# Optimization experiments

Hardware: AMD Instinct MI355X
Metric: run time of the kernel (lower is better)

## Reference

```python
import jax, jax.numpy as jnp
import numpy as np
from jax import lax

B, T = 64, 200
NUM_C, DIM_S, SIZE_M = 2000, 128, 50


def setup_inputs() -> dict:
    key = jax.random.key(0)
    ks = jax.random.split(key, 12)
    d = {}
    d['skill'] = jax.random.randint(ks[0], (B, T), 0, NUM_C)
    d['answer'] = jax.random.randint(ks[1], (B, T), 0, 2)
    s = 1.0 / np.sqrt(DIM_S)
    d['k_emb'] = jax.random.normal(ks[2], (NUM_C + 1, DIM_S), jnp.float32)
    d['v_emb'] = jax.random.normal(ks[3], (2 * NUM_C + 1, DIM_S), jnp.float32)
    # kaiming_normal on [size_m, dim_s]: std = sqrt(2/dim_s)
    d['Mk'] = jax.random.normal(ks[4], (SIZE_M, DIM_S), jnp.float32) * np.sqrt(2.0 / DIM_S)
    d['Mv0'] = jax.random.normal(ks[5], (SIZE_M, DIM_S), jnp.float32) * np.sqrt(2.0 / DIM_S)
    d['f_W'] = jax.random.normal(ks[6], (DIM_S, 2 * DIM_S), jnp.float32) * (1.0 / np.sqrt(2 * DIM_S))
    d['f_b'] = jnp.zeros((DIM_S,), jnp.float32)
    d['p_W'] = jax.random.normal(ks[7], (NUM_C, DIM_S), jnp.float32) * s
    d['p_b'] = jnp.zeros((NUM_C,), jnp.float32)
    d['e_W'] = jax.random.normal(ks[8], (DIM_S, DIM_S), jnp.float32) * s
    d['e_b'] = jnp.zeros((DIM_S,), jnp.float32)
    d['a_W'] = jax.random.normal(ks[9], (DIM_S, DIM_S), jnp.float32) * s
    d['a_b'] = jnp.zeros((DIM_S,), jnp.float32)
    return d


def reference(skill, answer, k_emb, v_emb, Mk, Mv0, f_W, f_b, p_W, p_b, e_W, e_b, a_W, a_b):
    num_c = p_W.shape[0]
    bsz = skill.shape[0]
    answer_x = jnp.where(answer == 2, 1, answer)
    x = skill + num_c * answer_x                       # [B,T]
    k = k_emb[skill]                                   # [B,T,D]
    v = v_emb[x]                                       # [B,T,D]
    w = jax.nn.softmax(jnp.einsum('btd,md->btm', k, Mk), axis=-1)   # [B,T,M]
    e = jax.nn.sigmoid(jnp.einsum('btd,ed->bte', v, e_W) + e_b)      # [B,T,D]
    a = jnp.tanh(jnp.einsum('btd,ed->bte', v, a_W) + a_b)            # [B,T,D]

    Mv_init = jnp.broadcast_to(Mv0, (bsz,) + Mv0.shape)              # [B,M,D]

    def step(Mvt, inp):
        et, at, wt = inp                               # [B,D],[B,D],[B,M]
        # read uses pre-update memory (Mv[:, :-1] in the torch code)
        read = jnp.einsum('bm,bmd->bd', wt, Mvt)
        Mvt_new = Mvt * (1.0 - wt[:, :, None] * et[:, None, :]) + wt[:, :, None] * at[:, None, :]
        return Mvt_new, read

    _, reads = lax.scan(step, Mv_init,
                        (e.transpose(1, 0, 2), a.transpose(1, 0, 2), w.transpose(1, 0, 2)))
    reads = reads.transpose(1, 0, 2)                   # [B,T,D]

    f = jnp.tanh(jnp.concatenate([reads, k], axis=-1) @ f_W.T + f_b)  # [B,T,D]
    p = jax.nn.sigmoid(f @ p_W.T + p_b)                # [B,T,num_c] (dropout is identity at eval)
    p = p[:, :-1, :]
    next_skill = skill[:, 1:]                          # [B,T-1]
    idx = jnp.minimum(next_skill, num_c - 1)
    pred = jnp.take_along_axis(p, idx[..., None], axis=-1)[..., 0]
    pred = jnp.where(next_skill < num_c, pred, 0.0)    # index num_c -> zero row in torch one_hot
    return pred
```

## Files before the change

### kernel.cpp

```cpp
#include <hip/hip_runtime.h>
#include <math.h>

#define Bsz 64
#define Tn 200
#define NUMC 2000
#define DS 128
#define SM 50
#define NTOK (Bsz*Tn)
#define WG2 10
#define MPG2 5

typedef __attribute__((ext_vector_type(8))) short bfrag;
typedef __attribute__((ext_vector_type(4))) float f32x4;
typedef __attribute__((ext_vector_type(4))) unsigned int u32x4;

__device__ __forceinline__ unsigned short f2bf(float x) {
    unsigned int u = __builtin_bit_cast(unsigned int, x);
    u = u + 0x7fffu + ((u >> 16) & 1u);
    return (unsigned short)(u >> 16);
}
__device__ __forceinline__ unsigned int pack2(float a, float b) {
    return (unsigned int)f2bf(a) | ((unsigned int)f2bf(b) << 16);
}
__device__ __forceinline__ bfrag mk_frag(f32x4 x, f32x4 y) {
    u32x4 t;
    t[0] = pack2(x[0], x[1]); t[1] = pack2(x[2], x[3]);
    t[2] = pack2(y[0], y[1]); t[3] = pack2(y[2], y[3]);
    return __builtin_bit_cast(bfrag, t);
}

__device__ __forceinline__ float fast_exp(float x)  { return __builtin_amdgcn_exp2f(x * 1.44269504f); }
__device__ __forceinline__ float fast_rcp(float x)  { return __builtin_amdgcn_rcpf(x); }
__device__ __forceinline__ float fast_sigmoid(float x) { return fast_rcp(1.f + fast_exp(-x)); }
__device__ __forceinline__ float fast_tanh(float x) { return 1.f - 2.f * fast_rcp(fast_exp(2.f * x) + 1.f); }

__device__ __forceinline__ void load_group(const bfrag* __restrict__ B, int nt0, int L, bfrag bf[4][4]) {
    #pragma unroll
    for (int t = 0; t < 4; t++)
        #pragma unroll
        for (int ki = 0; ki < 4; ki++)
            bf[t][ki] = B[(size_t)((nt0 + t) * 4 + ki) * 64 + L];
}
__device__ __forceinline__ void mfma_group(const bfrag A[4], const bfrag bf[4][4], f32x4 acc[4]) {
    #pragma unroll
    for (int ki = 0; ki < 4; ki++)
        #pragma unroll
        for (int t = 0; t < 4; t++)
            acc[t] = __builtin_amdgcn_mfma_f32_16x16x32_bf16(A[ki], bf[t][ki], acc[t], 0, 0, 0);
}

__global__ __launch_bounds__(256) void k0_cast(
    const float* __restrict__ eW, const float* __restrict__ aW,
    const float* __restrict__ fW, const float* __restrict__ Mk,
    unsigned int* __restrict__ BeaU, unsigned int* __restrict__ BkmU,
    unsigned int* __restrict__ Bf0U)
{
    const int g = blockIdx.x * 256 + threadIdx.x;
    if (g >= 9216) return;
    int gm, mat;
    unsigned int* dst;
    if (g < 4096)      { mat = 0; gm = g;        dst = BeaU; }
    else if (g < 7168) { mat = 1; gm = g - 4096; dst = BkmU; }
    else               { mat = 2; gm = g - 7168; dst = Bf0U; }
    const int nt = gm >> 8, r = gm & 255, ki = r >> 6, L = r & 63;
    const int n = nt * 16 + (L & 15);
    const int k = ki * 32 + (L >> 4) * 8;

    const float* src = nullptr;
    if (mat == 0) {
        src = (n < 128) ? (eW + (size_t)n * DS + k) : (aW + (size_t)(n - 128) * DS + k);
    } else if (mat == 1) {
        if (n < 128)      src = fW + (size_t)n * (2 * DS) + DS + k;
        else if (n < 128 + SM) src = Mk + (size_t)(n - 128) * DS + k;
    } else {
        src = fW + (size_t)n * (2 * DS) + k;
    }
    float v[8];
    #pragma unroll
    for (int j = 0; j < 8; j++) v[j] = src ? src[j] : 0.f;
    u32x4 o;
    o[0] = pack2(v[0], v[1]); o[1] = pack2(v[2], v[3]);
    o[2] = pack2(v[4], v[5]); o[3] = pack2(v[6], v[7]);
    ((u32x4*)dst)[gm] = o;
}

__global__ __launch_bounds__(64) void k1_gemm(
    const int* __restrict__ skill, const int* __restrict__ answer,
    const float* __restrict__ k_emb, const float* __restrict__ v_emb,
    const unsigned int* __restrict__ BeaU, const unsigned int* __restrict__ BkmU,
    const float* __restrict__ eB, const float* __restrict__ aB,
    float* __restrict__ w_buf, float* __restrict__ e_buf,
    float* __restrict__ a_buf, float* __restrict__ kp_buf)
{
    const int bid = blockIdx.x;
    const int L = threadIdx.x, L15 = L & 15, quad = L >> 4;

    if (bid < NTOK/16) {
        const int tok0 = bid * 16;
        const int tokA = tok0 + L15;
        const int tokD0 = tok0 + quad * 4;

        const bfrag* Bea = (const bfrag*)BeaU;
        bfrag bfA[4][4], bfB[4][4];
        load_group(Bea, 0, L, bfA);
        load_group(Bea, 4, L, bfB);

        const int s  = skill[tokA];
        const int an = answer[tokA];
        const int ax = (an == 2) ? 1 : an;
        const float* vp = v_emb + ((size_t)(s + NUMC * ax)) * DS + quad * 8;
        bfrag Vf[4];
        #pragma unroll
        for (int ki = 0; ki < 4; ki++) {
            const f32x4* a = (const f32x4*)(vp + ki * 32);
            Vf[ki] = mk_frag(a[0], a[1]);
        }

        f32x4 acc[4];
        #pragma unroll
        for (int t = 0; t < 4; t++) acc[t] = (f32x4){0.f,0.f,0.f,0.f};
        mfma_group(Vf, bfA, acc);
        load_group(Bea, 8, L, bfA);
        #pragma unroll
        for (int t = 0; t < 4; t++) {
            const int n = t * 16 + L15;
            const float bias = eB[n];
            #pragma unroll
            for (int reg = 0; reg < 4; reg++)
                e_buf[(size_t)(tokD0 + reg) * DS + n] = fast_sigmoid(acc[t][reg] + bias);
        }

        #pragma unroll
        for (int t = 0; t < 4; t++) acc[t] = (f32x4){0.f,0.f,0.f,0.f};
        mfma_group(Vf, bfB, acc);
        load_group(Bea, 12, L, bfB);
        #pragma unroll
        for (int t = 0; t < 4; t++) {
            const int n = (4 + t) * 16 + L15;
            const float bias = eB[n];
            #pragma unroll
            for (int reg = 0; reg < 4; reg++)
                e_buf[(size_t)(tokD0 + reg) * DS + n] = fast_sigmoid(acc[t][reg] + bias);
        }

        #pragma unroll
        for (int t = 0; t < 4; t++) acc[t] = (f32x4){0.f,0.f,0.f,0.f};
        mfma_group(Vf, bfA, acc);
        #pragma unroll
        for (int t = 0; t < 4; t++) {
            const int n = t * 16 + L15;
            const float bias = aB[n];
            #pragma unroll
            for (int reg = 0; reg < 4; reg++)
                a_buf[(size_t)(tokD0 + reg) * DS + n] = fast_tanh(acc[t][reg] + bias);
        }

        #pragma unroll
        for (int t = 0; t < 4; t++) acc[t] = (f32x4){0.f,0.f,0.f,0.f};
        mfma_group(Vf, bfB, acc);
        #pragma unroll
        for (int t = 0; t < 4; t++) {
            const int n = (4 + t) * 16 + L15;
            const float bias = aB[n];
            #pragma unroll
            for (int reg = 0; reg < 4; reg++)
                a_buf[(size_t)(tokD0 + reg) * DS + n] = fast_tanh(acc[t][reg] + bias);
        }
    } else {
        const int tok0 = (bid - NTOK/16) * 16;
        const int tokA = tok0 + L15;
        const int tokD0 = tok0 + quad * 4;

        const bfrag* Bkm = (const bfrag*)BkmU;
        bfrag bfA[4][4], bfB[4][4];
        load_group(Bkm, 0, L, bfA);
        load_group(Bkm, 4, L, bfB);

        const int s = skill[tokA];
        const float* kp = k_emb + (size_t)s * DS + quad * 8;
        bfrag Kf[4];
        #pragma unroll
        for (int ki = 0; ki < 4; ki++) {
            const f32x4* b = (const f32x4*)(kp + ki * 32);
            Kf[ki] = mk_frag(b[0], b[1]);
        }

        __shared__ float wl[16][52];

        f32x4 acc[4];
        #pragma unroll
        for (int t = 0; t < 4; t++) acc[t] = (f32x4){0.f,0.f,0.f,0.f};
        mfma_group(Kf, bfA, acc);
        load_group(Bkm, 8, L, bfA);
        #pragma unroll
        for (int t = 0; t < 4; t++) {
            const int n = t * 16 + L15;
            #pragma unroll
            for (int reg = 0; reg < 4; reg++)
                kp_buf[(size_t)(tokD0 + reg) * DS + n] = acc[t][reg];
        }

        #pragma unroll
        for (int t = 0; t < 4; t++) acc[t] = (f32x4){0.f,0.f,0.f,0.f};
        mfma_group(Kf, bfB, acc);
        #pragma unroll
        for (int t = 0; t < 4; t++) {
            const int n = (4 + t) * 16 + L15;
            #pragma unroll
            for (int reg = 0; reg < 4; reg++)
                kp_buf[(size_t)(tokD0 + reg) * DS + n] = acc[t][reg];
        }

        #pragma unroll
        for (int t = 0; t < 4; t++) acc[t] = (f32x4){0.f,0.f,0.f,0.f};
        mfma_group(Kf, bfA, acc);
        #pragma unroll
        for (int t = 0; t < 4; t++) {
            const int c = (8 + t) * 16 + L15 - 128;
            if (c < SM) {
                #pragma unroll
                for (int reg = 0; reg < 4; reg++)
                    wl[quad * 4 + reg][c] = acc[t][reg];
            }
        }
        __syncthreads();
        if (L < 16) {
            float mx = -1e30f;
            for (int m = 0; m < SM; m++) mx = fmaxf(mx, wl[L][m]);
            float sum = 0.f;
            float ex[SM];
            for (int m = 0; m < SM; m++) { ex[m] = fast_exp(wl[L][m] - mx); sum += ex[m]; }
            const float inv = fast_rcp(sum);
            float* wp = w_buf + (size_t)(tok0 + L) * SM;
            for (int m = 0; m < SM; m++) wp[m] = ex[m] * inv;
        }
    }
}

__global__ __launch_bounds__(64) void k2_scan(
    const float* __restrict__ w_buf, const float* __restrict__ e_buf,
    const float* __restrict__ a_buf, const float* __restrict__ Mv0,
    float* __restrict__ part_buf)
{
    const int bi   = blockIdx.x;
    const int b    = bi / (2*WG2);
    const int r    = bi % (2*WG2);
    const int dh   = r / WG2;
    const int mg   = r % WG2;
    const int lane = threadIdx.x;
    const int d    = dh*64 + lane;
    const int m0   = mg * MPG2;
    const int base = b * Tn;

    float Mv[MPG2];
    #pragma unroll
    for (int m = 0; m < MPG2; m++) Mv[m] = Mv0[(size_t)(m0+m)*DS + d];

    float* pout = part_buf + (size_t)mg * NTOK * DS;

    float se[4][2], sa[4][2], sw[4][2][MPG2];

    #define LOADST(ST, T)                                                      \
        { const int tc_ = ((T) < Tn) ? (T) : 0;                                \
          _Pragma("unroll")                                                    \
          for (int q_ = 0; q_ < 2; q_++) {                                     \
              const int tf_ = base + tc_ + q_;                                 \
              se[ST][q_] = e_buf[(size_t)tf_*DS + d];                          \
              sa[ST][q_] = a_buf[(size_t)tf_*DS + d];                          \
              _Pragma("unroll")                                                \
              for (int m_ = 0; m_ < MPG2; m_++)                                \
                  sw[ST][q_][m_] = w_buf[(size_t)tf_*SM + m0 + m_];            \
          } }

    LOADST(0, 0) LOADST(1, 2) LOADST(2, 4) LOADST(3, 6)

    for (int i = 0; i < 25; i++) {
        const int tb = i * 8;
        #pragma unroll
        for (int sub = 0; sub < 4; sub++) {
            const int t0 = tb + sub * 2;
            #pragma unroll
            for (int q = 0; q < 2; q++) {
                const float ev = se[sub][q], av = sa[sub][q];
                float rd = 0.f;
                #pragma unroll
                for (int m = 0; m < MPG2; m++) {
                    const float wm = sw[sub][q][m];
                    rd = fmaf(wm, Mv[m], rd);
                    Mv[m] = fmaf(-wm, fmaf(ev, Mv[m], -av), Mv[m]);
                }
                pout[(size_t)(base + t0 + q)*DS + d] = rd;
            }
            LOADST(sub, t0 + 8)
        }
    }
}

__global__ __launch_bounds__(64) void k3_gemm(
    const float* __restrict__ part_buf, const float* __restrict__ kp_buf,
    const unsigned int* __restrict__ Bf0U, const float* __restrict__ fB,
    const float* __restrict__ pW, const float* __restrict__ pB,
    const int* __restrict__ skill, float* __restrict__ out)
{
    const int L = threadIdx.x, L15 = L & 15, quad = L >> 4;
    const int tok0 = blockIdx.x * 16;
    const int tokA = tok0 + L15;
    const int tokD0 = tok0 + quad * 4;

    const bfrag* Bf0 = (const bfrag*)Bf0U;
    bfrag bfA[4][4], bfB[4][4];
    load_group(Bf0, 0, L, bfA);
    load_group(Bf0, 4, L, bfB);

    bfrag Rf[4];
    #pragma unroll
    for (int ki = 0; ki < 4; ki++) {
        const float* p0 = part_buf + (size_t)tokA * DS + ki * 32 + quad * 8;
        f32x4 x = (f32x4){0.f,0.f,0.f,0.f}, y = (f32x4){0.f,0.f,0.f,0.f};
        #pragma unroll
        for (int g = 0; g < WG2; g++) {
            const f32x4* q4 = (const f32x4*)(p0 + (size_t)g * NTOK * DS);
            x = x + q4[0]; y = y + q4[1];
        }
        Rf[ki] = mk_frag(x, y);
    }

    float f[4][8];
    f32x4 acc[4];

    #pragma unroll
    for (int t = 0; t < 4; t++) acc[t] = (f32x4){0.f,0.f,0.f,0.f};
    mfma_group(Rf, bfA, acc);
    #pragma unroll
    for (int t = 0; t < 4; t++) {
        const int n = t * 16 + L15;
        const float fb = fB[n];
        #pragma unroll
        for (int reg = 0; reg < 4; reg++)
            f[reg][t] = fast_tanh(acc[t][reg] + kp_buf[(size_t)(tokD0 + reg) * DS + n] + fb);
    }

    #pragma unroll
    for (int t = 0; t < 4; t++) acc[t] = (f32x4){0.f,0.f,0.f,0.f};
    mfma_group(Rf, bfB, acc);
    #pragma unroll
    for (int t = 0; t < 4; t++) {
        const int n = (4 + t) * 16 + L15;
        const float fb = fB[n];
        #pragma unroll
        for (int reg = 0; reg < 4; reg++)
            f[reg][4 + t] = fast_tanh(acc[t][reg] + kp_buf[(size_t)(tokD0 + reg) * DS + n] + fb);
    }

    #pragma unroll
    for (int reg = 0; reg < 4; reg++) {
        const int tok = tokD0 + reg;
        const int t = tok % Tn;
        const bool act = (t < Tn - 1);
        int sn = 0, ix = 0;
        float contrib = 0.f;
        if (act) {
            sn = skill[tok + 1];
            ix = (sn < NUMC) ? sn : (NUMC - 1);
            const float* pr = pW + (size_t)ix * DS + L15;
            #pragma unroll
            for (int nt = 0; nt < 8; nt++)
                contrib = fmaf(f[reg][nt], pr[nt * 16], contrib);
        }
        #pragma unroll
        for (int msk = 1; msk <= 8; msk <<= 1)
            contrib += __shfl_xor(contrib, msk);
        if (act && L15 == 0) {
            const float val = contrib + pB[ix];
            const float prd = (sn < NUMC) ? fast_sigmoid(val) : 0.f;
            out[(size_t)(tok / Tn) * (Tn - 1) + t] = prd;
        }
    }
}

extern "C" void kernel_launch(void* const* d_in, const int* in_sizes, int n_in,
                              void* d_out, int out_size, void* d_ws, size_t ws_size,
                              hipStream_t stream)
{
    const int*   skill  = (const int*)  d_in[0];
    const int*   answer = (const int*)  d_in[1];
    const float* k_emb  = (const float*)d_in[2];
    const float* v_emb  = (const float*)d_in[3];
    const float* Mk     = (const float*)d_in[4];
    const float* Mv0    = (const float*)d_in[5];
    const float* f_W    = (const float*)d_in[6];
    const float* f_b    = (const float*)d_in[7];
    const float* p_W    = (const float*)d_in[8];
    const float* p_b    = (const float*)d_in[9];
    const float* e_W    = (const float*)d_in[10];
    const float* e_b    = (const float*)d_in[11];
    const float* a_W    = (const float*)d_in[12];
    const float* a_b    = (const float*)d_in[13];
    float* out = (float*)d_out;

    float* ws       = (float*)d_ws;
    float* w_buf    = ws;
    float* e_buf    = w_buf    + (size_t)NTOK*SM;
    float* a_buf    = e_buf    + (size_t)NTOK*DS;
    float* kp_buf   = a_buf    + (size_t)NTOK*DS;
    float* part_buf = kp_buf   + (size_t)NTOK*DS;
    unsigned int* BeaU = (unsigned int*)(part_buf + (size_t)WG2*NTOK*DS);
    unsigned int* BkmU = BeaU + 4096 * 4;
    unsigned int* Bf0U = BkmU + 3072 * 4;

    k0_cast<<<36, 256, 0, stream>>>(e_W, a_W, f_W, Mk, BeaU, BkmU, Bf0U);
    k1_gemm<<<2*(NTOK/16), 64, 0, stream>>>(skill, answer, k_emb, v_emb,
        BeaU, BkmU, e_b, a_b, w_buf, e_buf, a_buf, kp_buf);
    k2_scan<<<Bsz*2*WG2, 64, 0, stream>>>(w_buf, e_buf, a_buf, Mv0, part_buf);
    k3_gemm<<<NTOK/16, 64, 0, stream>>>(part_buf, kp_buf, Bf0U, f_b,
        p_W, p_b, skill, out);
}
```

Measured before the change: 140.6 us.

## Fuse all stages into one cooperative kernel with grid syncs and bf16 partials

Replaces the four separate launches (weight cast, projection GEMMs, memory scan, output GEMM) with one cooperative kernel of 256 blocks x 512 threads. Stages are separated by grid.sync, and each wave takes one work item. The softmax for w is now done in registers instead of through LDS. The scan's per-group partial reads are stored as bf16 rather than fp32, halving partial-buffer traffic. In exchange the stages are serialized by grid barriers, occupancy depends on the cooperative grid size, and the partials lose some precision.

Measured after the change: 232.3 us. 65.2% more time.

```diff
diff --git a/kernel.cpp b/kernel.cpp
--- a/kernel.cpp
+++ b/kernel.cpp
@@ -1,5 +1,8 @@
 #include <hip/hip_runtime.h>
+#include <hip/hip_cooperative_groups.h>
 #include <math.h>
+
+namespace cg = cooperative_groups;
 
 #define Bsz 64
 #define Tn 200
@@ -22,6 +25,9 @@
 __device__ __forceinline__ unsigned int pack2(float a, float b) {
     return (unsigned int)f2bf(a) | ((unsigned int)f2bf(b) << 16);
 }
+__device__ __forceinline__ float bf2f(unsigned int u) {
+    return __builtin_bit_cast(float, u << 16);
+}
 __device__ __forceinline__ bfrag mk_frag(f32x4 x, f32x4 y) {
     u32x4 t;
     t[0] = pack2(x[0], x[1]); t[1] = pack2(x[2], x[3]);
@@ -49,331 +55,346 @@
             acc[t] = __builtin_amdgcn_mfma_f32_16x16x32_bf16(A[ki], bf[t][ki], acc[t], 0, 0, 0);
 }
 
-__global__ __launch_bounds__(256) void k0_cast(
-    const float* __restrict__ eW, const float* __restrict__ aW,
-    const float* __restrict__ fW, const float* __restrict__ Mk,
+__global__ __launch_bounds__(512, 2) void fused(
+    const int* __restrict__ skill, const int* __restrict__ answer,
+    const float* __restrict__ k_emb, const float* __restrict__ v_emb,
+    const float* __restrict__ Mk, const float* __restrict__ Mv0,
+    const float* __restrict__ fW, const float* __restrict__ fB,
+    const float* __restrict__ pW, const float* __restrict__ pB,
+    const float* __restrict__ eW, const float* __restrict__ eB,
+    const float* __restrict__ aW, const float* __restrict__ aB,
+    float* __restrict__ out,
+    float* __restrict__ w_buf, float* __restrict__ e_buf,
+    float* __restrict__ a_buf, float* __restrict__ kp_buf,
+    unsigned short* __restrict__ part16,
     unsigned int* __restrict__ BeaU, unsigned int* __restrict__ BkmU,
     unsigned int* __restrict__ Bf0U)
 {
-    const int g = blockIdx.x * 256 + threadIdx.x;
-    if (g >= 9216) return;
-    int gm, mat;
-    unsigned int* dst;
-    if (g < 4096)      { mat = 0; gm = g;        dst = BeaU; }
-    else if (g < 7168) { mat = 1; gm = g - 4096; dst = BkmU; }
-    else               { mat = 2; gm = g - 7168; dst = Bf0U; }
-    const int nt = gm >> 8, r = gm & 255, ki = r >> 6, L = r & 63;
-    const int n = nt * 16 + (L & 15);
-    const int k = ki * 32 + (L >> 4) * 8;
-
-    const float* src = nullptr;
-    if (mat == 0) {
-        src = (n < 128) ? (eW + (size_t)n * DS + k) : (aW + (size_t)(n - 128) * DS + k);
-    } else if (mat == 1) {
-        if (n < 128)      src = fW + (size_t)n * (2 * DS) + DS + k;
-        else if (n < 128 + SM) src = Mk + (size_t)(n - 128) * DS + k;
-    } else {
-        src = fW + (size_t)n * (2 * DS) + k;
-    }
-    float v[8];
-    #pragma unroll
-    for (int j = 0; j < 8; j++) v[j] = src ? src[j] : 0.f;
-    u32x4 o;
-    o[0] = pack2(v[0], v[1]); o[1] = pack2(v[2], v[3]);
-    o[2] = pack2(v[4], v[5]); o[3] = pack2(v[6], v[7]);
-    ((u32x4*)dst)[gm] = o;
-}
-
-__global__ __launch_bounds__(64) void k1_gemm(
-    const int* __restrict__ skill, const int* __restrict__ answer,
-    const float* __restrict__ k_emb, const float* __restrict__ v_emb,
-    const unsigned int* __restrict__ BeaU, const unsigned int* __restrict__ BkmU,
-    const float* __restrict__ eB, const float* __restrict__ aB,
-    float* __restrict__ w_buf, float* __restrict__ e_buf,
-    float* __restrict__ a_buf, float* __restrict__ kp_buf)
-{
-    const int bid = blockIdx.x;
-    const int L = threadIdx.x, L15 = L & 15, quad = L >> 4;
-
-    if (bid < NTOK/16) {
-        const int tok0 = bid * 16;
-        const int tokA = tok0 + L15;
-        const int tokD0 = tok0 + quad * 4;
-
-        const bfrag* Bea = (const bfrag*)BeaU;
-        bfrag bfA[4][4], bfB[4][4];
-        load_group(Bea, 0, L, bfA);
-        load_group(Bea, 4, L, bfB);
-
-        const int s  = skill[tokA];
-        const int an = answer[tokA];
-        const int ax = (an == 2) ? 1 : an;
-        const float* vp = v_emb + ((size_t)(s + NUMC * ax)) * DS + quad * 8;
-        bfrag Vf[4];
-        #pragma unroll
-        for (int ki = 0; ki < 4; ki++) {
-            const f32x4* a = (const f32x4*)(vp + ki * 32);
-            Vf[ki] = mk_frag(a[0], a[1]);
-        }
-
-        f32x4 acc[4];
-        #pragma unroll
-        for (int t = 0; t < 4; t++) acc[t] = (f32x4){0.f,0.f,0.f,0.f};
-        mfma_group(Vf, bfA, acc);
-        load_group(Bea, 8, L, bfA);
-        #pragma unroll
-        for (int t = 0; t < 4; t++) {
-            const int n = t * 16 + L15;
-            const float bias = eB[n];
-            #pragma unroll
-            for (int reg = 0; reg < 4; reg++)
-                e_buf[(size_t)(tokD0 + reg) * DS + n] = fast_sigmoid(acc[t][reg] + bias);
-        }
-
-        #pragma unroll
-        for (int t = 0; t < 4; t++) acc[t] = (f32x4){0.f,0.f,0.f,0.f};
-        mfma_group(Vf, bfB, acc);
-        load_group(Bea, 12, L, bfB);
-        #pragma unroll
-        for (int t = 0; t < 4; t++) {
-            const int n = (4 + t) * 16 + L15;
-            const float bias = eB[n];
-            #pragma unroll
-            for (int reg = 0; reg < 4; reg++)
-                e_buf[(size_t)(tokD0 + reg) * DS + n] = fast_sigmoid(acc[t][reg] + bias);
-        }
-
-        #pragma unroll
-        for (int t = 0; t < 4; t++) acc[t] = (f32x4){0.f,0.f,0.f,0.f};
-        mfma_group(Vf, bfA, acc);
-        #pragma unroll
-        for (int t = 0; t < 4; t++) {
-            const int n = t * 16 + L15;
-            const float bias = aB[n];
-            #pragma unroll
-            for (int reg = 0; reg < 4; reg++)
-                a_buf[(size_t)(tokD0 + reg) * DS + n] = fast_tanh(acc[t][reg] + bias);
-        }
-
-        #pragma unroll
-        for (int t = 0; t < 4; t++) acc[t] = (f32x4){0.f,0.f,0.f,0.f};
-        mfma_group(Vf, bfB, acc);
-        #pragma unroll
-        for (int t = 0; t < 4; t++) {
-            const int n = (4 + t) * 16 + L15;
-            const float bias = aB[n];
-            #pragma unroll
-            for (int reg = 0; reg < 4; reg++)
-                a_buf[(size_t)(tokD0 + reg) * DS + n] = fast_tanh(acc[t][reg] + bias);
-        }
-    } else {
-        const int tok0 = (bid - NTOK/16) * 16;
-        const int tokA = tok0 + L15;
-        const int tokD0 = tok0 + quad * 4;
-
-        const bfrag* Bkm = (const bfrag*)BkmU;
-        bfrag bfA[4][4], bfB[4][4];
-        load_group(Bkm, 0, L, bfA);
-        load_group(Bkm, 4, L, bfB);
-
-        const int s = skill[tokA];
-        const float* kp = k_emb + (size_t)s * DS + quad * 8;
-        bfrag Kf[4];
-        #pragma unroll
-        for (int ki = 0; ki < 4; ki++) {
-            const f32x4* b = (const f32x4*)(kp + ki * 32);
-            Kf[ki] = mk_frag(b[0], b[1]);
-        }
-
-        __shared__ float wl[16][52];
-
-        f32x4 acc[4];
-        #pragma unroll
-        for (int t = 0; t < 4; t++) acc[t] = (f32x4){0.f,0.f,0.f,0.f};
-        mfma_group(Kf, bfA, acc);
-        load_group(Bkm, 8, L, bfA);
-        #pragma unroll
-        for (int t = 0; t < 4; t++) {
-            const int n = t * 16 + L15;
-            #pragma unroll
-            for (int reg = 0; reg < 4; reg++)
-                kp_buf[(size_t)(tokD0 + reg) * DS + n] = acc[t][reg];
-        }
-
-        #pragma unroll
-        for (int t = 0; t < 4; t++) acc[t] = (f32x4){0.f,0.f,0.f,0.f};
-        mfma_group(Kf, bfB, acc);
-        #pragma unroll
-        for (int t = 0; t < 4; t++) {
-            const int n = (4 + t) * 16 + L15;
-            #pragma unroll
-            for (int reg = 0; reg < 4; reg++)
-                kp_buf[(size_t)(tokD0 + reg) * DS + n] = acc[t][reg];
-        }
-
-        #pragma unroll
-        for (int t = 0; t < 4; t++) acc[t] = (f32x4){0.f,0.f,0.f,0.f};
-        mfma_group(Kf, bfA, acc);
-        #pragma unroll
-        for (int t = 0; t < 4; t++) {
-            const int c = (8 + t) * 16 + L15 - 128;
-            if (c < SM) {
-                #pragma unroll
-                for (int reg = 0; reg < 4; reg++)
-                    wl[quad * 4 + reg][c] = acc[t][reg];
-            }
-        }
-        __syncthreads();
-        if (L < 16) {
-            float mx = -1e30f;
-            for (int m = 0; m < SM; m++) mx = fmaxf(mx, wl[L][m]);
-            float sum = 0.f;
-            float ex[SM];
-            for (int m = 0; m < SM; m++) { ex[m] = fast_exp(wl[L][m] - mx); sum += ex[m]; }
-            const float inv = fast_rcp(sum);
-            float* wp = w_buf + (size_t)(tok0 + L) * SM;
-            for (int m = 0; m < SM; m++) wp[m] = ex[m] * inv;
+    cg::grid_group grid = cg::this_grid();
+    const int tid = threadIdx.x;
+    const int wv  = tid >> 6;
+    const int L   = tid & 63, L15 = L & 15, quad = (L >> 4) & 3;
+
+    {
+        const int g = blockIdx.x * 512 + tid;
+        if (g < 9216) {
+            int gm, mat;
+            unsigned int* dst;
+            if (g < 4096)      { mat = 0; gm = g;        dst = BeaU; }
+            else if (g < 7168) { mat = 1; gm = g - 4096; dst = BkmU; }
+            else               { mat = 2; gm = g - 7168; dst = Bf0U; }
+            const int nt = gm >> 8, r = gm & 255, ki = r >> 6, Lc = r & 63;
+            const int n = nt * 16 + (Lc & 15);
+            const int k = ki * 32 + (Lc >> 4) * 8;
+            const float* src = nullptr;
+            if (mat == 0) {
+                src = (n < 128) ? (eW + (size_t)n * DS + k) : (aW + (size_t)(n - 128) * DS + k);
+            } else if (mat == 1) {
+                if (n < 128)           src = fW + (size_t)n * (2 * DS) + DS + k;
+                else if (n < 128 + SM) src = Mk + (size_t)(n - 128) * DS + k;
+            } else {
+                src = fW + (size_t)n * (2 * DS) + k;
+            }
+            float v[8];
+            #pragma unroll
+            for (int j = 0; j < 8; j++) v[j] = src ? src[j] : 0.f;
+            u32x4 o;
+            o[0] = pack2(v[0], v[1]); o[1] = pack2(v[2], v[3]);
+            o[2] = pack2(v[4], v[5]); o[3] = pack2(v[6], v[7]);
+            ((u32x4*)dst)[gm] = o;
         }
     }
-}
-
-__global__ __launch_bounds__(64) void k2_scan(
-    const float* __restrict__ w_buf, const float* __restrict__ e_buf,
-    const float* __restrict__ a_buf, const float* __restrict__ Mv0,
-    float* __restrict__ part_buf)
-{
-    const int bi   = blockIdx.x;
-    const int b    = bi / (2*WG2);
-    const int r    = bi % (2*WG2);
-    const int dh   = r / WG2;
-    const int mg   = r % WG2;
-    const int lane = threadIdx.x;
-    const int d    = dh*64 + lane;
-    const int m0   = mg * MPG2;
-    const int base = b * Tn;
-
-    float Mv[MPG2];
-    #pragma unroll
-    for (int m = 0; m < MPG2; m++) Mv[m] = Mv0[(size_t)(m0+m)*DS + d];
-
-    float* pout = part_buf + (size_t)mg * NTOK * DS;
-
-    float se[4][2], sa[4][2], sw[4][2][MPG2];
-
-    #define LOADST(ST, T)                                                      \
-        { const int tc_ = ((T) < Tn) ? (T) : 0;                                \
-          _Pragma("unroll")                                                    \
-          for (int q_ = 0; q_ < 2; q_++) {                                     \
-              const int tf_ = base + tc_ + q_;                                 \
-              se[ST][q_] = e_buf[(size_t)tf_*DS + d];                          \
-              sa[ST][q_] = a_buf[(size_t)tf_*DS + d];                          \
-              _Pragma("unroll")                                                \
-              for (int m_ = 0; m_ < MPG2; m_++)                                \
-                  sw[ST][q_][m_] = w_buf[(size_t)tf_*SM + m0 + m_];            \
-          } }
-
-    LOADST(0, 0) LOADST(1, 2) LOADST(2, 4) LOADST(3, 6)
-
-    for (int i = 0; i < 25; i++) {
-        const int tb = i * 8;
-        #pragma unroll
-        for (int sub = 0; sub < 4; sub++) {
-            const int t0 = tb + sub * 2;
-            #pragma unroll
-            for (int q = 0; q < 2; q++) {
-                const float ev = se[sub][q], av = sa[sub][q];
-                float rd = 0.f;
-                #pragma unroll
-                for (int m = 0; m < MPG2; m++) {
-                    const float wm = sw[sub][q][m];
-                    rd = fmaf(wm, Mv[m], rd);
-                    Mv[m] = fmaf(-wm, fmaf(ev, Mv[m], -av), Mv[m]);
-                }
-                pout[(size_t)(base + t0 + q)*DS + d] = rd;
-            }
-            LOADST(sub, t0 + 8)
+    grid.sync();
+
+    {
+        const int tA = wv * 256 + blockIdx.x;
+        if (tA < 800) {
+            const int tok0 = tA * 16;
+            const int tokA = tok0 + L15;
+            const int tokD0 = tok0 + quad * 4;
+
+            const bfrag* Bea = (const bfrag*)BeaU;
+            bfrag bfA[4][4], bfB[4][4];
+            load_group(Bea, 0, L, bfA);
+            load_group(Bea, 4, L, bfB);
+
+            const int s  = skill[tokA];
+            const int an = answer[tokA];
+            const int ax = (an == 2) ? 1 : an;
+            const float* vp = v_emb + ((size_t)(s + NUMC * ax)) * DS + quad * 8;
+            bfrag Vf[4];
+            #pragma unroll
+            for (int ki = 0; ki < 4; ki++) {
+                const f32x4* a = (const f32x4*)(vp + ki * 32);
+                Vf[ki] = mk_frag(a[0], a[1]);
+            }
+
+            f32x4 acc[4];
+            #pragma unroll
+            for (int t = 0; t < 4; t++) acc[t] = (f32x4){0.f,0.f,0.f,0.f};
+            mfma_group(Vf, bfA, acc);
+            load_group(Bea, 8, L, bfA);
+            #pragma unroll
+            for (int t = 0; t < 4; t++) {
+                const int n = t * 16 + L15;
+                const float bias = eB[n];
+                #pragma unroll
+                for (int reg = 0; reg < 4; reg++)
+                    e_buf[(size_t)(tokD0 + reg) * DS + n] = fast_sigmoid(acc[t][reg] + bias);
+            }
+
+            #pragma unroll
+            for (int t = 0; t < 4; t++) acc[t] = (f32x4){0.f,0.f,0.f,0.f};
+            mfma_group(Vf, bfB, acc);
+            load_group(Bea, 12, L, bfB);
+            #pragma unroll
+            for (int t = 0; t < 4; t++) {
+                const int n = (4 + t) * 16 + L15;
+                const float bias = eB[n];
+                #pragma unroll
+                for (int reg = 0; reg < 4; reg++)
+                    e_buf[(size_t)(tokD0 + reg) * DS + n] = fast_sigmoid(acc[t][reg] + bias);
+            }
+
+            #pragma unroll
+            for (int t = 0; t < 4; t++) acc[t] = (f32x4){0.f,0.f,0.f,0.f};
+            mfma_group(Vf, bfA, acc);
+            #pragma unroll
+            for (int t = 0; t < 4; t++) {
+                const int n = t * 16 + L15;
+                const float bias = aB[n];
+                #pragma unroll
+                for (int reg = 0; reg < 4; reg++)
+                    a_buf[(size_t)(tokD0 + reg) * DS + n] = fast_tanh(acc[t][reg] + bias);
+            }
+
+            #pragma unroll
+            for (int t = 0; t < 4; t++) acc[t] = (f32x4){0.f,0.f,0.f,0.f};
+            mfma_group(Vf, bfB, acc);
+            #pragma unroll
+            for (int t = 0; t < 4; t++) {
+                const int n = (4 + t) * 16 + L15;
+                const float bias = aB[n];
+                #pragma unroll
+                for (int reg = 0; reg < 4; reg++)
+                    a_buf[(size_t)(tokD0 + reg) * DS + n] = fast_tanh(acc[t][reg] + bias);
+            }
+        } else if (tA < 1600) {
+            const int tok0 = (tA - 800) * 16;
+            const int tokA = tok0 + L15;
+            const int tokD0 = tok0 + quad * 4;
+
+            const bfrag* Bkm = (const bfrag*)BkmU;
+            bfrag bfA[4][4], bfB[4][4];
+            load_group(Bkm, 0, L, bfA);
+            load_group(Bkm, 4, L, bfB);
+
+            const int s = skill[tokA];
+            const float* kp = k_emb + (size_t)s * DS + quad * 8;
+            bfrag Kf[4];
+            #pragma unroll
+            for (int ki = 0; ki < 4; ki++) {
+                const f32x4* b = (const f32x4*)(kp + ki * 32);
+                Kf[ki] = mk_frag(b[0], b[1]);
+            }
+
+            f32x4 acc[4];
+            #pragma unroll
+            for (int t = 0; t < 4; t++) acc[t] = (f32x4){0.f,0.f,0.f,0.f};
+            mfma_group(Kf, bfA, acc);
+            load_group(Bkm, 8, L, bfA);
+            #pragma unroll
+            for (int t = 0; t < 4; t++) {
+                const int n = t * 16 + L15;
+                #pragma unroll
+                for (int reg = 0; reg < 4; reg++)
+                    kp_buf[(size_t)(tokD0 + reg) * DS + n] = acc[t][reg];
+            }
+
+            #pragma unroll
+            for (int t = 0; t < 4; t++) acc[t] = (f32x4){0.f,0.f,0.f,0.f};
+            mfma_group(Kf, bfB, acc);
+            #pragma unroll
+            for (int t = 0; t < 4; t++) {
+                const int n = (4 + t) * 16 + L15;
+                #pragma unroll
+                for (int reg = 0; reg < 4; reg++)
+                    kp_buf[(size_t)(tokD0 + reg) * DS + n] = acc[t][reg];
+            }
+
+            #pragma unroll
+            for (int t = 0; t < 4; t++) acc[t] = (f32x4){0.f,0.f,0.f,0.f};
+            mfma_group(Kf, bfA, acc);
+            #pragma unroll
+            for (int reg = 0; reg < 4; reg++) {
+                float mx = -1e30f;
+                #pragma unroll
+                for (int t = 0; t < 4; t++) {
+                    const int c = t * 16 + L15;
+                    if (c < SM) mx = fmaxf(mx, acc[t][reg]);
+                }
+                #pragma unroll
+                for (int msk = 1; msk <= 8; msk <<= 1)
+                    mx = fmaxf(mx, __shfl_xor(mx, msk));
+                float ex[4], sum = 0.f;
+                #pragma unroll
+                for (int t = 0; t < 4; t++) {
+                    const int c = t * 16 + L15;
+                    ex[t] = (c < SM) ? fast_exp(acc[t][reg] - mx) : 0.f;
+                    sum += ex[t];
+                }
+                #pragma unroll
+                for (int msk = 1; msk <= 8; msk <<= 1)
+                    sum += __shfl_xor(sum, msk);
+                const float inv = fast_rcp(sum);
+                float* wp = w_buf + (size_t)(tok0 + quad * 4 + reg) * SM;
+                #pragma unroll
+                for (int t = 0; t < 4; t++) {
+                    const int c = t * 16 + L15;
+                    if (c < SM) wp[c] = ex[t] * inv;
+                }
+            }
         }
     }
-}
-
-__global__ __launch_bounds__(64) void k3_gemm(
-    const float* __restrict__ part_buf, const float* __restrict__ kp_buf,
-    const unsigned int* __restrict__ Bf0U, const float* __restrict__ fB,
-    const float* __restrict__ pW, const float* __restrict__ pB,
-    const int* __restrict__ skill, float* __restrict__ out)
-{
-    const int L = threadIdx.x, L15 = L & 15, quad = L >> 4;
-    const int tok0 = blockIdx.x * 16;
-    const int tokA = tok0 + L15;
-    const int tokD0 = tok0 + quad * 4;
-
-    const bfrag* Bf0 = (const bfrag*)Bf0U;
-    bfrag bfA[4][4], bfB[4][4];
-    load_group(Bf0, 0, L, bfA);
-    load_group(Bf0, 4, L, bfB);
-
-    bfrag Rf[4];
-    #pragma unroll
-    for (int ki = 0; ki < 4; ki++) {
-        const float* p0 = part_buf + (size_t)tokA * DS + ki * 32 + quad * 8;
-        f32x4 x = (f32x4){0.f,0.f,0.f,0.f}, y = (f32x4){0.f,0.f,0.f,0.f};
-        #pragma unroll
-        for (int g = 0; g < WG2; g++) {
-            const f32x4* q4 = (const f32x4*)(p0 + (size_t)g * NTOK * DS);
-            x = x + q4[0]; y = y + q4[1];
+    grid.sync();
+
+    {
+        const int bi = blockIdx.x * 5 + wv;
+        if (wv < 5) {
+            const int b    = bi / (2*WG2);
+            const int r    = bi % (2*WG2);
+            const int dh   = r / WG2;
+            const int mg   = r % WG2;
+            const int d    = dh*64 + L;
+            const int m0   = mg * MPG2;
+            const int base = b * Tn;
+
+            float Mv[MPG2];
+            #pragma unroll
+            for (int m = 0; m < MPG2; m++) Mv[m] = Mv0[(size_t)(m0+m)*DS + d];
+
+            unsigned short* pout = part16 + (size_t)mg * NTOK * DS;
+
+            float se[4][2], sa[4][2], sw[4][2][MPG2];
+
+            #define LOADST(ST, T)                                                      \
+                { const int tc_ = ((T) < Tn) ? (T) : 0;                                \
+                  _Pragma("unroll")                                                    \
+                  for (int q_ = 0; q_ < 2; q_++) {                                     \
+                      const int tf_ = base + tc_ + q_;                                 \
+                      se[ST][q_] = e_buf[(size_t)tf_*DS + d];                          \
+                      sa[ST][q_] = a_buf[(size_t)tf_*DS + d];                          \
+                      _Pragma("unroll")                                                \
+                      for (int m_ = 0; m_ < MPG2; m_++)                                \
+                          sw[ST][q_][m_] = w_buf[(size_t)tf_*SM + m0 + m_];            \
+                  } }
+
+            LOADST(0, 0) LOADST(1, 2) LOADST(2, 4) LOADST(3, 6)
+
+            for (int i = 0; i < 25; i++) {
+                const int tb = i * 8;
+                #pragma unroll
+                for (int sub = 0; sub < 4; sub++) {
+                    const int t0 = tb + sub * 2;
+                    #pragma unroll
+                    for (int q = 0; q < 2; q++) {
+                        const float ev = se[sub][q], av = sa[sub][q];
+                        float rd = 0.f;
+                        #pragma unroll
+                        for (int m = 0; m < MPG2; m++) {
+                            const float wm = sw[sub][q][m];
+                            rd = fmaf(wm, Mv[m], rd);
+                            Mv[m] = fmaf(-wm, fmaf(ev, Mv[m], -av), Mv[m]);
+                        }
+                        pout[(size_t)(base + t0 + q)*DS + d] = f2bf(rd);
+                    }
+                    LOADST(sub, t0 + 8)
+                }
+            }
+            #undef LOADST
         }
-        Rf[ki] = mk_frag(x, y);
     }
-
-    float f[4][8];
-    f32x4 acc[4];
-
-    #pragma unroll
-    for (int t = 0; t < 4; t++) acc[t] = (f32x4){0.f,0.f,0.f,0.f};
-    mfma_group(Rf, bfA, acc);
-    #pragma unroll
-    for (int t = 0; t < 4; t++) {
-        const int n = t * 16 + L15;
-        const float fb = fB[n];
-        #pragma unroll
-        for (int reg = 0; reg < 4; reg++)
-            f[reg][t] = fast_tanh(acc[t][reg] + kp_buf[(size_t)(tokD0 + reg) * DS + n] + fb);
-    }
-
-    #pragma unroll
-    for (int t = 0; t < 4; t++) acc[t] = (f32x4){0.f,0.f,0.f,0.f};
-    mfma_group(Rf, bfB, acc);
-    #pragma unroll
-    for (int t = 0; t < 4; t++) {
-        const int n = (4 + t) * 16 + L15;
-        const float fb = fB[n];
-        #pragma unroll
-        for (int reg = 0; reg < 4; reg++)
-            f[reg][4 + t] = fast_tanh(acc[t][reg] + kp_buf[(size_t)(tokD0 + reg) * DS + n] + fb);
-    }
-
-    #pragma unroll
-    for (int reg = 0; reg < 4; reg++) {
-        const int tok = tokD0 + reg;
-        const int t = tok % Tn;
-        const bool act = (t < Tn - 1);
-        int sn = 0, ix = 0;
-        float contrib = 0.f;
-        if (act) {
-            sn = skill[tok + 1];
-            ix = (sn < NUMC) ? sn : (NUMC - 1);
-            const float* pr = pW + (size_t)ix * DS + L15;
-            #pragma unroll
-            for (int nt = 0; nt < 8; nt++)
-                contrib = fmaf(f[reg][nt], pr[nt * 16], contrib);
-        }
-        #pragma unroll
-        for (int msk = 1; msk <= 8; msk <<= 1)
-            contrib += __shfl_xor(contrib, msk);
-        if (act && L15 == 0) {
-            const float val = contrib + pB[ix];
-            const float prd = (sn < NUMC) ? fast_sigmoid(val) : 0.f;
-            out[(size_t)(tok / Tn) * (Tn - 1) + t] = prd;
+    grid.sync();
+
+    {
+        const int tC = wv * 256 + blockIdx.x;
+        if (tC < 800) {
+            const int tok0 = tC * 16;
+            const int tokA = tok0 + L15;
+            const int tokD0 = tok0 + quad * 4;
+
+            const bfrag* Bf0 = (const bfrag*)Bf0U;
+            bfrag bfA[4][4], bfB[4][4];
+            load_group(Bf0, 0, L, bfA);
+            load_group(Bf0, 4, L, bfB);
+
+            bfrag Rf[4];
+            #pragma unroll
+            for (int ki = 0; ki < 4; ki++) {
+                const unsigned short* p0 = part16 + (size_t)tokA * DS + ki * 32 + quad * 8;
+                float s0=0,s1=0,s2=0,s3=0,s4=0,s5=0,s6=0,s7=0;
+                #pragma unroll
+                for (int g = 0; g < WG2; g++) {
+                    u32x4 v = *(const u32x4*)(p0 + (size_t)g * NTOK * DS);
+                    s0 += bf2f(v[0] & 0xffffu); s1 += bf2f(v[0] >> 16);
+                    s2 += bf2f(v[1] & 0xffffu); s3 += bf2f(v[1] >> 16);
+                    s4 += bf2f(v[2] & 0xffffu); s5 += bf2f(v[2] >> 16);
+                    s6 += bf2f(v[3] & 0xffffu); s7 += bf2f(v[3] >> 16);
+                }
+                Rf[ki] = mk_frag((f32x4){s0,s1,s2,s3}, (f32x4){s4,s5,s6,s7});
+            }
+
+            float f[4][8];
+            f32x4 acc[4];
+
+            #pragma unroll
+            for (int t = 0; t < 4; t++) acc[t] = (f32x4){0.f,0.f,0.f,0.f};
+            mfma_group(Rf, bfA, acc);
+            #pragma unroll
+            for (int t = 0; t < 4; t++) {
+                const int n = t * 16 + L15;
+                const float fb = fB[n];
+                #pragma unroll
+                for (int reg = 0; reg < 4; reg++)
+                    f[reg][t] = fast_tanh(acc[t][reg] + kp_buf[(size_t)(tokD0 + reg) * DS + n] + fb);
+            }
+
+            #pragma unroll
+            for (int t = 0; t < 4; t++) acc[t] = (f32x4){0.f,0.f,0.f,0.f};
+            mfma_group(Rf, bfB, acc);
+            #pragma unroll
+            for (int t = 0; t < 4; t++) {
+                const int n = (4 + t) * 16 + L15;
+                const float fb = fB[n];
+                #pragma unroll
+                for (int reg = 0; reg < 4; reg++)
+                    f[reg][4 + t] = fast_tanh(acc[t][reg] + kp_buf[(size_t)(tokD0 + reg) * DS + n] + fb);
+            }
+
+            #pragma unroll
+            for (int reg = 0; reg < 4; reg++) {
+                const int tok = tokD0 + reg;
+                const int t = tok % Tn;
+                const bool act = (t < Tn - 1);
+                int sn = 0, ix = 0;
+                float contrib = 0.f;
+                if (act) {
+                    sn = skill[tok + 1];
+                    ix = (sn < NUMC) ? sn : (NUMC - 1);
+                    const float* pr = pW + (size_t)ix * DS + L15;
+                    #pragma unroll
+                    for (int nt = 0; nt < 8; nt++)
+                        contrib = fmaf(f[reg][nt], pr[nt * 16], contrib);
+                }
+                #pragma unroll
+                for (int msk = 1; msk <= 8; msk <<= 1)
+                    contrib += __shfl_xor(contrib, msk);
+                if (act && L15 == 0) {
+                    const float val = contrib + pB[ix];
+                    const float prd = (sn < NUMC) ? fast_sigmoid(val) : 0.f;
+                    out[(size_t)(tok / Tn) * (Tn - 1) + t] = prd;
+                }
+            }
         }
     }
 }
@@ -398,20 +419,23 @@
     const float* a_b    = (const float*)d_in[13];
     float* out = (float*)d_out;
 
-    float* ws       = (float*)d_ws;
-    float* w_buf    = ws;
-    float* e_buf    = w_buf    + (size_t)NTOK*SM;
-    float* a_buf    = e_buf    + (size_t)NTOK*DS;
-    float* kp_buf   = a_buf    + (size_t)NTOK*DS;
-    float* part_buf = kp_buf   + (size_t)NTOK*DS;
-    unsigned int* BeaU = (unsigned int*)(part_buf + (size_t)WG2*NTOK*DS);
+    float* ws     = (float*)d_ws;
+    float* w_buf  = ws;
+    float* e_buf  = w_buf  + (size_t)NTOK*SM;
+    float* a_buf  = e_buf  + (size_t)NTOK*DS;
+    float* kp_buf = a_buf  + (size_t)NTOK*DS;
+    unsigned short* part16 = (unsigned short*)(kp_buf + (size_t)NTOK*DS);
+    unsigned int* BeaU = (unsigned int*)(part16 + (size_t)WG2*NTOK*DS);
     unsigned int* BkmU = BeaU + 4096 * 4;
     unsigned int* Bf0U = BkmU + 3072 * 4;
 
-    k0_cast<<<36, 256, 0, stream>>>(e_W, a_W, f_W, Mk, BeaU, BkmU, Bf0U);
-    k1_gemm<<<2*(NTOK/16), 64, 0, stream>>>(skill, answer, k_emb, v_emb,
-        BeaU, BkmU, e_b, a_b, w_buf, e_buf, a_buf, kp_buf);
-    k2_scan<<<Bsz*2*WG2, 64, 0, stream>>>(w_buf, e_buf, a_buf, Mv0, part_buf);
-    k3_gemm<<<NTOK/16, 64, 0, stream>>>(part_buf, kp_buf, Bf0U, f_b,
-        p_W, p_b, skill, out);
-}
+    void* args[] = {
+        (void*)&skill, (void*)&answer, (void*)&k_emb, (void*)&v_emb,
+        (void*)&Mk, (void*)&Mv0, (void*)&f_W, (void*)&f_b,
+        (void*)&p_W, (void*)&p_b, (void*)&e_W, (void*)&e_b,
+        (void*)&a_W, (void*)&a_b, (void*)&out,
+        (void*)&w_buf, (void*)&e_buf, (void*)&a_buf, (void*)&kp_buf,
+        (void*)&part16, (void*)&BeaU, (void*)&BkmU, (void*)&Bf0U
+    };
+    hipLaunchCooperativeKernel((void*)fused, dim3(256), dim3(512), args, 0, stream);
+}
```

## Interleave e/a buffers, pad softmax weights per group, deepen scan prefetch

Applied to the files above, without the earlier changes.

The k1 softmax now runs in registers with cross-lane shuffles instead of going through shared memory with only 16 threads active. Its output goes to a padded 80-float-per-token layout grouped by memory slot, so the scan can fetch each group's weights with one vector load plus one scalar. e and a are stored interleaved so the scan reads both with one 8-byte load. The scan's prefetch depth doubles from 8 to 16 timesteps, and a launch bound hint of two blocks is added. The aim is fewer load instructions and more latency hiding in the serial scan, at the cost of more registers and a larger w buffer.

After: 155.3 us. 10.5% more time.

```diff
diff --git a/kernel.cpp b/kernel.cpp
--- a/kernel.cpp
+++ b/kernel.cpp
@@ -12,6 +12,7 @@
 
 typedef __attribute__((ext_vector_type(8))) short bfrag;
 typedef __attribute__((ext_vector_type(4))) float f32x4;
+typedef __attribute__((ext_vector_type(2))) float f32x2;
 typedef __attribute__((ext_vector_type(4))) unsigned int u32x4;
 
 __device__ __forceinline__ unsigned short f2bf(float x) {
@@ -70,7 +71,7 @@
     if (mat == 0) {
         src = (n < 128) ? (eW + (size_t)n * DS + k) : (aW + (size_t)(n - 128) * DS + k);
     } else if (mat == 1) {
-        if (n < 128)      src = fW + (size_t)n * (2 * DS) + DS + k;
+        if (n < 128)           src = fW + (size_t)n * (2 * DS) + DS + k;
         else if (n < 128 + SM) src = Mk + (size_t)(n - 128) * DS + k;
     } else {
         src = fW + (size_t)n * (2 * DS) + k;
@@ -89,8 +90,7 @@
     const float* __restrict__ k_emb, const float* __restrict__ v_emb,
     const unsigned int* __restrict__ BeaU, const unsigned int* __restrict__ BkmU,
     const float* __restrict__ eB, const float* __restrict__ aB,
-    float* __restrict__ w_buf, float* __restrict__ e_buf,
-    float* __restrict__ a_buf, float* __restrict__ kp_buf)
+    float* __restrict__ w2, float* __restrict__ ea_buf, float* __restrict__ kp_buf)
 {
     const int bid = blockIdx.x;
     const int L = threadIdx.x, L15 = L & 15, quad = L >> 4;
@@ -127,7 +127,7 @@
             const float bias = eB[n];
             #pragma unroll
             for (int reg = 0; reg < 4; reg++)
-                e_buf[(size_t)(tokD0 + reg) * DS + n] = fast_sigmoid(acc[t][reg] + bias);
+                ea_buf[(size_t)(tokD0 + reg) * (2*DS) + 2*n] = fast_sigmoid(acc[t][reg] + bias);
         }
 
         #pragma unroll
@@ -140,7 +140,7 @@
             const float bias = eB[n];
             #pragma unroll
             for (int reg = 0; reg < 4; reg++)
-                e_buf[(size_t)(tokD0 + reg) * DS + n] = fast_sigmoid(acc[t][reg] + bias);
+                ea_buf[(size_t)(tokD0 + reg) * (2*DS) + 2*n] = fast_sigmoid(acc[t][reg] + bias);
         }
 
         #pragma unroll
@@ -152,7 +152,7 @@
             const float bias = aB[n];
             #pragma unroll
             for (int reg = 0; reg < 4; reg++)
-                a_buf[(size_t)(tokD0 + reg) * DS + n] = fast_tanh(acc[t][reg] + bias);
+                ea_buf[(size_t)(tokD0 + reg) * (2*DS) + 2*n + 1] = fast_tanh(acc[t][reg] + bias);
         }
 
         #pragma unroll
@@ -164,7 +164,7 @@
             const float bias = aB[n];
             #pragma unroll
             for (int reg = 0; reg < 4; reg++)
-                a_buf[(size_t)(tokD0 + reg) * DS + n] = fast_tanh(acc[t][reg] + bias);
+                ea_buf[(size_t)(tokD0 + reg) * (2*DS) + 2*n + 1] = fast_tanh(acc[t][reg] + bias);
         }
     } else {
         const int tok0 = (bid - NTOK/16) * 16;
@@ -185,8 +185,6 @@
             Kf[ki] = mk_frag(b[0], b[1]);
         }
 
-        __shared__ float wl[16][52];
-
         f32x4 acc[4];
         #pragma unroll
         for (int t = 0; t < 4; t++) acc[t] = (f32x4){0.f,0.f,0.f,0.f};
@@ -215,32 +213,40 @@
         for (int t = 0; t < 4; t++) acc[t] = (f32x4){0.f,0.f,0.f,0.f};
         mfma_group(Kf, bfA, acc);
         #pragma unroll
-        for (int t = 0; t < 4; t++) {
-            const int c = (8 + t) * 16 + L15 - 128;
-            if (c < SM) {
-                #pragma unroll
-                for (int reg = 0; reg < 4; reg++)
-                    wl[quad * 4 + reg][c] = acc[t][reg];
+        for (int reg = 0; reg < 4; reg++) {
+            float mx = -1e30f;
+            #pragma unroll
+            for (int t = 0; t < 4; t++) {
+                const int c = t * 16 + L15;
+                if (c < SM) mx = fmaxf(mx, acc[t][reg]);
             }
-        }
-        __syncthreads();
-        if (L < 16) {
-            float mx = -1e30f;
-            for (int m = 0; m < SM; m++) mx = fmaxf(mx, wl[L][m]);
-            float sum = 0.f;
-            float ex[SM];
-            for (int m = 0; m < SM; m++) { ex[m] = fast_exp(wl[L][m] - mx); sum += ex[m]; }
+            #pragma unroll
+            for (int msk = 1; msk <= 8; msk <<= 1)
+                mx = fmaxf(mx, __shfl_xor(mx, msk));
+            float ex[4], sum = 0.f;
+            #pragma unroll
+            for (int t = 0; t < 4; t++) {
+                const int c = t * 16 + L15;
+                ex[t] = (c < SM) ? fast_exp(acc[t][reg] - mx) : 0.f;
+                sum += ex[t];
+            }
+            #pragma unroll
+            for (int msk = 1; msk <= 8; msk <<= 1)
+                sum += __shfl_xor(sum, msk);
             const float inv = fast_rcp(sum);
-            float* wp = w_buf + (size_t)(tok0 + L) * SM;
-            for (int m = 0; m < SM; m++) wp[m] = ex[m] * inv;
-        }
-    }
-}
-
-__global__ __launch_bounds__(64) void k2_scan(
-    const float* __restrict__ w_buf, const float* __restrict__ e_buf,
-    const float* __restrict__ a_buf, const float* __restrict__ Mv0,
-    float* __restrict__ part_buf)
+            float* wp = w2 + (size_t)(tok0 + quad * 4 + reg) * 80;
+            #pragma unroll
+            for (int t = 0; t < 4; t++) {
+                const int c = t * 16 + L15;
+                if (c < SM) wp[(c / MPG2) * 8 + (c % MPG2)] = ex[t] * inv;
+            }
+        }
+    }
+}
+
+__global__ __launch_bounds__(64, 2) void k2_scan(
+    const float* __restrict__ w2, const float* __restrict__ ea_buf,
+    const float* __restrict__ Mv0, float* __restrict__ part_buf)
 {
     const int bi   = blockIdx.x;
     const int b    = bi / (2*WG2);
@@ -258,42 +264,48 @@
 
     float* pout = part_buf + (size_t)mg * NTOK * DS;
 
-    float se[4][2], sa[4][2], sw[4][2][MPG2];
-
-    #define LOADST(ST, T)                                                      \
-        { const int tc_ = ((T) < Tn) ? (T) : 0;                                \
-          _Pragma("unroll")                                                    \
-          for (int q_ = 0; q_ < 2; q_++) {                                     \
-              const int tf_ = base + tc_ + q_;                                 \
-              se[ST][q_] = e_buf[(size_t)tf_*DS + d];                          \
-              sa[ST][q_] = a_buf[(size_t)tf_*DS + d];                          \
-              _Pragma("unroll")                                                \
-              for (int m_ = 0; m_ < MPG2; m_++)                                \
-                  sw[ST][q_][m_] = w_buf[(size_t)tf_*SM + m0 + m_];            \
+    f32x2 rea[8][2];
+    float rw[8][2][MPG2];
+
+    #define LOADST(ST, T)                                                          \
+        { const int tc_ = ((T) < Tn) ? (T) : 0;                                    \
+          _Pragma("unroll")                                                        \
+          for (int q_ = 0; q_ < 2; q_++) {                                         \
+              const int tf_ = base + tc_ + q_;                                     \
+              rea[ST][q_] = *(const f32x2*)(ea_buf + (size_t)tf_*(2*DS) + 2*d);    \
+              const float* wp_ = w2 + (size_t)tf_*80 + mg*8;                       \
+              f32x4 w4_ = *(const f32x4*)wp_;                                      \
+              rw[ST][q_][0]=w4_[0]; rw[ST][q_][1]=w4_[1];                          \
+              rw[ST][q_][2]=w4_[2]; rw[ST][q_][3]=w4_[3];                          \
+              rw[ST][q_][4]=wp_[4];                                               \
           } }
 
+    #define STAGE(ST, T0)                                                          \
+        { _Pragma("unroll")                                                        \
+          for (int q = 0; q < 2; q++) {                                            \
+              const float ev = rea[ST][q][0], av = rea[ST][q][1];                  \
+              float rd = 0.f;                                                      \
+              _Pragma("unroll")                                                    \
+              for (int m = 0; m < MPG2; m++) {                                     \
+                  const float wm = rw[ST][q][m];                                   \
+                  rd = fmaf(wm, Mv[m], rd);                            \
+                  Mv[m] = fmaf(-wm, fmaf(ev, Mv[m], -av), Mv[m]);      \
+              }                                                                    \
+              pout[(size_t)(base + (T0) + q)*DS + d] = rd;                         \
+          }                                                                        \
+          LOADST(ST, (T0) + 16) }
+
     LOADST(0, 0) LOADST(1, 2) LOADST(2, 4) LOADST(3, 6)
-
-    for (int i = 0; i < 25; i++) {
-        const int tb = i * 8;
-        #pragma unroll
-        for (int sub = 0; sub < 4; sub++) {
-            const int t0 = tb + sub * 2;
-            #pragma unroll
-            for (int q = 0; q < 2; q++) {
-                const float ev = se[sub][q], av = sa[sub][q];
-                float rd = 0.f;
-                #pragma unroll
-                for (int m = 0; m < MPG2; m++) {
-                    const float wm = sw[sub][q][m];
-                    rd = fmaf(wm, Mv[m], rd);
-                    Mv[m] = fmaf(-wm, fmaf(ev, Mv[m], -av), Mv[m]);
-                }
-                pout[(size_t)(base + t0 + q)*DS + d] = rd;
-            }
-            LOADST(sub, t0 + 8)
-        }
-    }
+    LOADST(4, 8) LOADST(5, 10) LOADST(6, 12) LOADST(7, 14)
+
+    for (int blk = 0; blk < 12; blk++) {
+        const int t0 = blk * 16;
+        STAGE(0, t0)      STAGE(1, t0 + 2)  STAGE(2, t0 + 4)  STAGE(3, t0 + 6)
+        STAGE(4, t0 + 8)  STAGE(5, t0 + 10) STAGE(6, t0 + 12) STAGE(7, t0 + 14)
+    }
+    STAGE(0, 192) STAGE(1, 194) STAGE(2, 196) STAGE(3, 198)
+    #undef STAGE
+    #undef LOADST
 }
 
 __global__ __launch_bounds__(64) void k3_gemm(
@@ -399,19 +411,18 @@
     float* out = (float*)d_out;
 
     float* ws       = (float*)d_ws;
-    float* w_buf    = ws;
-    float* e_buf    = w_buf    + (size_t)NTOK*SM;
-    float* a_buf    = e_buf    + (size_t)NTOK*DS;
-    float* kp_buf   = a_buf    + (size_t)NTOK*DS;
-    float* part_buf = kp_buf   + (size_t)NTOK*DS;
+    float* w2       = ws;
+    float* ea_buf   = w2     + (size_t)NTOK*80;
+    float* kp_buf   = ea_buf + (size_t)NTOK*2*DS;
+    float* part_buf = kp_buf + (size_t)NTOK*DS;
     unsigned int* BeaU = (unsigned int*)(part_buf + (size_t)WG2*NTOK*DS);
     unsigned int* BkmU = BeaU + 4096 * 4;
     unsigned int* Bf0U = BkmU + 3072 * 4;
 
     k0_cast<<<36, 256, 0, stream>>>(e_W, a_W, f_W, Mk, BeaU, BkmU, Bf0U);
     k1_gemm<<<2*(NTOK/16), 64, 0, stream>>>(skill, answer, k_emb, v_emb,
-        BeaU, BkmU, e_b, a_b, w_buf, e_buf, a_buf, kp_buf);
-    k2_scan<<<Bsz*2*WG2, 64, 0, stream>>>(w_buf, e_buf, a_buf, Mv0, part_buf);
+        BeaU, BkmU, e_b, a_b, w2, ea_buf, kp_buf);
+    k2_scan<<<Bsz*2*WG2, 64, 0, stream>>>(w2, ea_buf, Mv0, part_buf);
     k3_gemm<<<NTOK/16, 64, 0, stream>>>(part_buf, kp_buf, Bf0U, f_b,
         p_W, p_b, skill, out);
 }
```
